# Performance work log

Hardware: AMD Instinct MI355X
Metric: run time of the kernel (lower is better)

The kernel has to match this reference:

```python
import jax, jax.numpy as jnp
import numpy as np

D_MODEL = 1024
HEAD = 16
HEAD_DIM = D_MODEL // HEAD


def setup_inputs() -> dict:
    key = jax.random.key(0)
    ks = jax.random.split(key, 11)
    B, S = 2, 2048
    q = jax.random.normal(ks[0], (B, S, D_MODEL), dtype=jnp.float32)
    k = jax.random.normal(ks[1], (B, S, D_MODEL), dtype=jnp.float32)
    v = jax.random.normal(ks[2], (B, S, D_MODEL), dtype=jnp.float32)
    # nn.Linear-style params: weight [out, in], bias [out]
    w_scale = 1.0 / np.sqrt(D_MODEL)
    def lin(kk):
        kw, kb = jax.random.split(kk)
        W = jax.random.uniform(kw, (D_MODEL, D_MODEL), jnp.float32, -w_scale, w_scale)
        b = jax.random.uniform(kb, (D_MODEL,), jnp.float32, -w_scale, w_scale)
        return W, b
    Wq, bq = lin(ks[3])
    Wk, bk = lin(ks[4])
    Wv, bv = lin(ks[5])
    Wo, bo = lin(ks[6])
    return {"query": q, "key": k, "value": v,
            "Wq": Wq, "bq": bq, "Wk": Wk, "bk": bk,
            "Wv": Wv, "bv": bv, "Wo": Wo, "bo": bo}


def reference(query, key, value, Wq, bq, Wk, bk, Wv, bv, Wo, bo):
    B, S, _ = query.shape
    # QKV projections (nn.Linear: x @ W.T + b)
    q = query @ Wq.T + bq
    k = key @ Wk.T + bk
    v = value @ Wv.T + bv
    # b s (h d) -> b h s d
    def split_heads(t):
        return t.reshape(B, -1, HEAD, HEAD_DIM).transpose(0, 2, 1, 3)
    q, k, v = split_heads(q), split_heads(k), split_heads(v)
    # NOTE: original forward never applies self.scale, and its masked_fill is
    # non-inplace (result discarded), so scores are raw QK^T with no masking.
    scores = jnp.einsum('bhid,bhjd->bhij', q, k)
    attn = jax.nn.softmax(scores, axis=-1)
    out = jnp.einsum('bhij,bhjd->bhid', attn, v)
    # b h s d -> b s (h d)
    out = out.transpose(0, 2, 1, 3).reshape(B, S, D_MODEL)
    # output projection (dropout=0.0)
    return out @ Wo.T + bo
```

## Files before the change

### kernel.cpp

```cpp
#include <hip/hip_runtime.h>
#include <stdint.h>

#define DM   1024
#define SEQ  2048
#define NH   16
#define HD   64
#define SHIFT 14.0f

typedef _Float16 f16;
typedef f16   half8 __attribute__((ext_vector_type(8)));
typedef f16   half4 __attribute__((ext_vector_type(4)));
typedef float f32x4 __attribute__((ext_vector_type(4)));
typedef float f32x16 __attribute__((ext_vector_type(16)));
typedef unsigned int u32;
typedef u32 u32x4 __attribute__((ext_vector_type(4)));

__device__ __forceinline__ void gl_lds16(const void* g, void* l) {
  __builtin_amdgcn_global_load_lds(
      reinterpret_cast<__attribute__((address_space(1))) u32*>(reinterpret_cast<uintptr_t>(g)),
      reinterpret_cast<__attribute__((address_space(3))) u32*>(reinterpret_cast<uintptr_t>(l)),
      16, 0, 0);
}

__device__ __forceinline__ u32 pkrtz(float a, float b) {
  auto h = __builtin_amdgcn_cvt_pkrtz(a, b);
  return __builtin_bit_cast(u32, h);
}

__global__ __launch_bounds__(256) void cast_all(
    const float* __restrict__ q, const float* __restrict__ k, const float* __restrict__ v,
    const float* __restrict__ Wq, const float* __restrict__ Wk,
    const float* __restrict__ Wv, const float* __restrict__ Wo,
    f16* __restrict__ qh, f16* __restrict__ kh, f16* __restrict__ vh,
    f16* __restrict__ Wqh, f16* __restrict__ Wkh, f16* __restrict__ Wvh,
    f16* __restrict__ Woh) {
  int i = blockIdx.x * 256 + threadIdx.x;
  const float* s;
  f16* d;
  int off;
  float sc = 1.0f;
  if (i < 1572864) {
    int sel = i >> 19;
    off = i & 524287;
    s = sel == 0 ? q : sel == 1 ? k : v;
    d = sel == 0 ? qh : sel == 1 ? kh : vh;
  } else {
    int j = i - 1572864;
    int sel = j >> 17;
    off = j & 131071;
    s = sel == 0 ? Wq : sel == 1 ? Wk : sel == 2 ? Wv : Wo;
    d = sel == 0 ? Wqh : sel == 1 ? Wkh : sel == 2 ? Wvh : Woh;
    if (sel == 0) sc = 1.44269504f;
  }
  const float4* s4 = reinterpret_cast<const float4*>(s);
  float4 a = s4[2 * (size_t)off];
  float4 b = s4[2 * (size_t)off + 1];
  half8 o;
  o[0] = (f16)(sc * a.x); o[1] = (f16)(sc * a.y); o[2] = (f16)(sc * a.z); o[3] = (f16)(sc * a.w);
  o[4] = (f16)(sc * b.x); o[5] = (f16)(sc * b.y); o[6] = (f16)(sc * b.z); o[7] = (f16)(sc * b.w);
  *reinterpret_cast<half8*>(d + 8 * (size_t)off) = o;
}

#define XCD_DECODE_N64                                                         \
  int bid = blockIdx.x;                                                        \
  int xcd = bid & 7;                                                           \
  int idx = bid >> 3;                                               \
  int m0 = (xcd * 4 + (idx >> 4)) * 128;                                       \
  int n0 = (idx & 15) * 64;

__global__ __launch_bounds__(512) void gemm_qkv(
    const f16* __restrict__ A0, const f16* __restrict__ A1, const f16* __restrict__ A2,
    const f16* __restrict__ W0, const f16* __restrict__ W1, const f16* __restrict__ W2,
    const float* __restrict__ b0, const float* __restrict__ b1, const float* __restrict__ b2,
    f16* __restrict__ C0, f16* __restrict__ C1, f16* __restrict__ C2) {
  int z = blockIdx.z;
  const f16* A = (z == 0) ? A0 : (z == 1) ? A1 : A2;
  const f16* W = (z == 0) ? W0 : (z == 1) ? W1 : W2;
  const float* bias = (z == 0) ? b0 : (z == 1) ? b1 : b2;

  XCD_DECODE_N64

  __shared__ f16 As[2][128 * 64];
  __shared__ f16 Ws[2][64 * 64];

  int t = threadIdx.x;
  int w = t >> 6, lane = t & 63, lr = lane & 15, lk = lane >> 4;
  int wr = (w >> 1) * 32;
  int wc = (w & 1) * 32;
  int srow = t >> 3;
  int swc = (t & 7) ^ (srow & 7);
  const f16* ga = A + (size_t)(m0 + srow) * DM + swc * 8;
  const f16* gw = W + (size_t)(n0 + srow) * DM + swc * 8;

  f32x4 zero4 = {0.f, 0.f, 0.f, 0.f};
  f32x4 acc[2][2];
#pragma unroll
  for (int mb = 0; mb < 2; ++mb)
#pragma unroll
    for (int nb = 0; nb < 2; ++nb) acc[mb][nb] = zero4;

  gl_lds16(ga,                    &As[0][t * 8]);
  gl_lds16(ga + (size_t)64 * DM,  &As[0][4096 + t * 8]);
  gl_lds16(gw,                    &Ws[0][t * 8]);
  __syncthreads();

  for (int kt = 0; kt < DM / 64; ++kt) {
    int cur = kt & 1;
    if (kt + 1 < DM / 64) {
      int k0 = (kt + 1) * 64;
      gl_lds16(ga + k0,                   &As[cur ^ 1][t * 8]);
      gl_lds16(ga + k0 + (size_t)64 * DM, &As[cur ^ 1][4096 + t * 8]);
      gl_lds16(gw + k0,                   &Ws[cur ^ 1][t * 8]);
    }
#pragma unroll
    for (int ks = 0; ks < 2; ++ks) {
      half8 af[2], wf[2];
#pragma unroll
      for (int mb = 0; mb < 2; ++mb) {
        int R = wr + mb * 16 + lr;
        int c = (ks * 64 + lk * 16) ^ ((lr & 7) << 4);
        af[mb] = *reinterpret_cast<const half8*>(
            reinterpret_cast<const char*>(&As[cur][0]) + R * 128 + c);
      }
#pragma unroll
      for (int nb = 0; nb < 2; ++nb) {
        int R = wc + nb * 16 + lr;
        int c = (ks * 64 + lk * 16) ^ ((lr & 7) << 4);
        wf[nb] = *reinterpret_cast<const half8*>(
            reinterpret_cast<const char*>(&Ws[cur][0]) + R * 128 + c);
      }
#pragma unroll
      for (int mb = 0; mb < 2; ++mb)
#pragma unroll
        for (int nb = 0; nb < 2; ++nb)
          acc[mb][nb] = __builtin_amdgcn_mfma_f32_16x16x32_f16(af[mb], wf[nb], acc[mb][nb], 0, 0, 0);
    }
    __syncthreads();
  }

  float bscale = (z == 0) ? 1.44269504f : 1.0f;
  float bv[2];
#pragma unroll
  for (int nb = 0; nb < 2; ++nb) bv[nb] = bias[n0 + wc + nb * 16 + lr] * bscale;

  int lk4 = lk * 4;
  if (z == 2) {
#pragma unroll
    for (int mb = 0; mb < 2; ++mb)
#pragma unroll
      for (int nb = 0; nb < 2; ++nb) {
        int r0 = m0 + wr + mb * 16 + lk4;
        int c = n0 + wc + nb * 16 + lr;
        int b_ = r0 >> 11, s_ = r0 & 2047;
        int h_ = c >> 6, d_ = c & 63;
        f16* dst = C2 + (((size_t)(b_ * NH + h_) * HD + d_) * SEQ + s_);
        half4 hv;
#pragma unroll
        for (int j = 0; j < 4; ++j) hv[j] = (f16)(acc[mb][nb][j] + bv[nb]);
        *reinterpret_cast<half4*>(dst) = hv;
      }
  } else {
    f16* C = (z == 0) ? C0 : C1;
#pragma unroll
    for (int mb = 0; mb < 2; ++mb)
#pragma unroll
      for (int nb = 0; nb < 2; ++nb)
#pragma unroll
        for (int j = 0; j < 4; ++j) {
          int r = m0 + wr + mb * 16 + lk4 + j;
          int c = n0 + wc + nb * 16 + lr;
          C[(size_t)r * DM + c] = (f16)(acc[mb][nb][j] + bv[nb]);
        }
  }
}

__global__ __launch_bounds__(256) void gemm_out(
    const f16* __restrict__ A, const f16* __restrict__ W,
    const float* __restrict__ bias, float* __restrict__ C) {
  XCD_DECODE_N64

  __shared__ f16 As[2][128 * 64];
  __shared__ f16 Ws[2][64 * 64];
  int t = threadIdx.x;
  int w = t >> 6, lane = t & 63, lr = lane & 15, lk = lane >> 4;
  int wr = (w >> 1) * 64, wc = (w & 1) * 32;
  int rloc = 8 * w + (lane >> 3);
  int swc = (lane & 7) ^ (lane >> 3);
  const f16* ga = A + (size_t)(m0 + rloc) * DM + swc * 8;
  const f16* gw = W + (size_t)(n0 + rloc) * DM + swc * 8;
  f32x4 zero4 = {0.f, 0.f, 0.f, 0.f};
  f32x4 acc[4][2];
#pragma unroll
  for (int mb = 0; mb < 4; ++mb)
#pragma unroll
    for (int nb = 0; nb < 2; ++nb) acc[mb][nb] = zero4;

#pragma unroll
  for (int j = 0; j < 4; ++j)
    gl_lds16(ga + (size_t)(32 * j) * DM, &As[0][j * 2048 + t * 8]);
#pragma unroll
  for (int j = 0; j < 2; ++j)
    gl_lds16(gw + (size_t)(32 * j) * DM, &Ws[0][j * 2048 + t * 8]);
  __syncthreads();

  for (int kt = 0; kt < DM / 64; ++kt) {
    int cur = kt & 1;
    if (kt + 1 < DM / 64) {
      int k0 = (kt + 1) * 64;
#pragma unroll
      for (int j = 0; j < 4; ++j)
        gl_lds16(ga + (size_t)(32 * j) * DM + k0, &As[cur ^ 1][j * 2048 + t * 8]);
#pragma unroll
      for (int j = 0; j < 2; ++j)
        gl_lds16(gw + (size_t)(32 * j) * DM + k0, &Ws[cur ^ 1][j * 2048 + t * 8]);
    }
#pragma unroll
    for (int ks = 0; ks < 2; ++ks) {
      half8 af[4], wf[2];
#pragma unroll
      for (int mb = 0; mb < 4; ++mb) {
        int R = wr + mb * 16 + lr;
        int c = (ks * 64 + lk * 16) ^ ((lr & 7) << 4);
        af[mb] = *reinterpret_cast<const half8*>(
            reinterpret_cast<const char*>(&As[cur][0]) + R * 128 + c);
      }
#pragma unroll
      for (int nb = 0; nb < 2; ++nb) {
        int R = wc + nb * 16 + lr;
        int c = (ks * 64 + lk * 16) ^ ((lr & 7) << 4);
        wf[nb] = *reinterpret_cast<const half8*>(
            reinterpret_cast<const char*>(&Ws[cur][0]) + R * 128 + c);
      }
#pragma unroll
      for (int mb = 0; mb < 4; ++mb)
#pragma unroll
        for (int nb = 0; nb < 2; ++nb)
          acc[mb][nb] = __builtin_amdgcn_mfma_f32_16x16x32_f16(af[mb], wf[nb], acc[mb][nb], 0, 0, 0);
    }
    __syncthreads();
  }

  float bv[2];
#pragma unroll
  for (int nb = 0; nb < 2; ++nb) bv[nb] = bias[n0 + wc + nb * 16 + lr];
  int lk4 = lk * 4;
#pragma unroll
  for (int mb = 0; mb < 4; ++mb)
#pragma unroll
    for (int nb = 0; nb < 2; ++nb)
#pragma unroll
      for (int j = 0; j < 4; ++j) {
        int r = m0 + wr + mb * 16 + lk4 + j;
        int c = n0 + wc + nb * 16 + lr;
        C[(size_t)r * DM + c] = acc[mb][nb][j] + bv[nb];
      }
}

__global__ __launch_bounds__(512) void attn_fwd17(const f16* __restrict__ Qg,
                                                  const f16* __restrict__ Kg,
                                                  const f16* __restrict__ VTg,
                                                  f16* __restrict__ Og) {
  int bid = blockIdx.x;
  int xcd = bid & 7;
  int slot = bid >> 3;
  int qt = slot & 7;
  int gh = slot >> 3;
  int bh = xcd | (gh << 3);
  int b = bh >> 4, h = bh & 15;

  size_t baseq = (size_t)b * SEQ * DM + (size_t)h * HD;
  const f16* Kp = Kg + baseq;
  const f16* VTp = VTg + (size_t)bh * HD * SEQ;

  __shared__ f16 Kl[2][64 * 128];
  __shared__ f16 Vl[2][64 * 128];

  int t = threadIdx.x;
  int w = t >> 6, lane = t & 63;
  int l31 = lane & 31, lh = lane >> 5;
  int vrow = t >> 4, vcb = t & 15;

  int tt = t >> 4;
  int ku = t & 15;
  int ke = (2 * tt) & 15;
  int kx = ku ^ ke;
  int ksel = (kx >> 3) & 1;
  int kcc = ksel ? ((kx ^ 1) & 7) : kx;
  int kvbase = 2 * tt + ksel;
  const f16* gK = Kp + (size_t)kvbase * DM + kcc * 8;
  const f16* gV = VTp + (size_t)vrow * SEQ + ((vcb ^ vrow) & 15) * 8;
  f16* lK = &Kl[0][t * 8];
  f16* lV = &Vl[0][t * 8];
  const int KSTEP = 128 * DM;
  const int VSTEP = 128;
  const int LBK = 64 * 128;
  const int LBV = 64 * 128;

  int qs = qt * 256 + w * 32 + l31;
  const f16* Qrow = Qg + baseq + (size_t)qs * DM;
  half8 qf[4];
#pragma unroll
  for (int s = 0; s < 4; ++s)
    qf[s] = *reinterpret_cast<const half8*>(Qrow + s * 16 + lh * 8);

  auto stage = [&](int kt, int buf) {
    if (t < 256) {
      int ko = kt * KSTEP, vo = kt * VSTEP;
#pragma unroll
      for (int j = 0; j < 4; ++j)
        gl_lds16(gK + ko + (size_t)(32 * j) * DM, lK + buf * LBK + j * 2048);
#pragma unroll
      for (int j = 0; j < 4; ++j)
        gl_lds16(gV + vo + (size_t)(16 * j) * SEQ, lV + buf * LBV + j * 2048);
    }
  };
  auto readKf = [&](int buf, int nbk, int s) -> half8 {
    int kv = nbk * 32 + l31;
    int cc = s * 2 + lh;
    int u = (((kv & 1) << 3) | cc) ^ (kv & 15);
    return *reinterpret_cast<const half8*>(
        reinterpret_cast<const char*>(&Kl[buf][0]) + (kv >> 1) * 256 + (u << 4));
  };
  auto readVf = [&](int buf, int mb, int ks) -> half8 {
    int d = mb * 32 + l31;
    int c = (ks * 32 + lh * 16) ^ ((d & 15) << 4);
    return *reinterpret_cast<const half8*>(
        reinterpret_cast<const char*>(&Vl[buf][0]) + d * 256 + c);
  };

  f32x16 mShift, o0, o1;
#pragma unroll
  for (int i = 0; i < 16; ++i) {
    mShift[i] = -SHIFT;
    o0[i] = 0.f;
    o1[i] = 0.f;
  }
  float l_r = 0.f;

  stage(0, 0);
  __syncthreads();

  const int NT = SEQ / 128;
  for (int kt = 0; kt < NT; ++kt) {
    int cur = kt & 1;
    if (kt + 1 < NT) stage(kt + 1, cur ^ 1);

    __builtin_amdgcn_s_setprio(1);
    half8 k0 = readKf(cur, 0, 0);
    half8 k1 = readKf(cur, 1, 0);
    half8 k2 = readKf(cur, 2, 0);
    half8 k3 = readKf(cur, 3, 0);
    f32x16 s0 = __builtin_amdgcn_mfma_f32_32x32x16_f16(k0, qf[0], mShift, 0, 0, 0);
    f32x16 s1 = __builtin_amdgcn_mfma_f32_32x32x16_f16(k1, qf[0], mShift, 0, 0, 0);
    f32x16 s2 = __builtin_amdgcn_mfma_f32_32x32x16_f16(k2, qf[0], mShift, 0, 0, 0);
    f32x16 s3 = __builtin_amdgcn_mfma_f32_32x32x16_f16(k3, qf[0], mShift, 0, 0, 0);
#pragma unroll
    for (int s = 1; s < 4; ++s) {
      k0 = readKf(cur, 0, s);
      k1 = readKf(cur, 1, s);
      k2 = readKf(cur, 2, s);
      k3 = readKf(cur, 3, s);
      s0 = __builtin_amdgcn_mfma_f32_32x32x16_f16(k0, qf[s], s0, 0, 0, 0);
      s1 = __builtin_amdgcn_mfma_f32_32x32x16_f16(k1, qf[s], s1, 0, 0, 0);
      s2 = __builtin_amdgcn_mfma_f32_32x32x16_f16(k2, qf[s], s2, 0, 0, 0);
      s3 = __builtin_amdgcn_mfma_f32_32x32x16_f16(k3, qf[s], s3, 0, 0, 0);
    }
    __builtin_amdgcn_s_setprio(0);

    float rs0 = 0.f, rs1 = 0.f, rs2 = 0.f, rs3 = 0.f;
#pragma unroll
    for (int i = 0; i < 16; ++i) { s0[i] = __builtin_amdgcn_exp2f(s0[i]); rs0 += s0[i]; }
#pragma unroll
    for (int i = 0; i < 16; ++i) { s1[i] = __builtin_amdgcn_exp2f(s1[i]); rs1 += s1[i]; }
#pragma unroll
    for (int i = 0; i < 16; ++i) { s2[i] = __builtin_amdgcn_exp2f(s2[i]); rs2 += s2[i]; }
#pragma unroll
    for (int i = 0; i < 16; ++i) { s3[i] = __builtin_amdgcn_exp2f(s3[i]); rs3 += s3[i]; }
    l_r += (rs0 + rs1) + (rs2 + rs3);

#define PVSTEP(SP, NBK)                                                        \
    {                                                                          \
      u32 u0 = pkrtz(SP[0], SP[1]);                                            \
      u32 u1 = pkrtz(SP[2], SP[3]);                                            \
      u32 u2 = pkrtz(SP[4], SP[5]);                                            \
      u32 u3 = pkrtz(SP[6], SP[7]);                                            \
      u32 u4 = pkrtz(SP[8], SP[9]);                                            \
      u32 u5 = pkrtz(SP[10], SP[11]);                                          \
      u32 u6 = pkrtz(SP[12], SP[13]);                                          \
      u32 u7 = pkrtz(SP[14], SP[15]);                                          \
      asm volatile("v_permlane32_swap_b32 %0, %1" : "+v"(u0), "+v"(u2));       \
      asm volatile("v_permlane32_swap_b32 %0, %1" : "+v"(u1), "+v"(u3));       \
      asm volatile("v_permlane32_swap_b32 %0, %1" : "+v"(u4), "+v"(u6));       \
      asm volatile("v_permlane32_swap_b32 %0, %1" : "+v"(u5), "+v"(u7));       \
      u32x4 w0 = {u0, u1, u2, u3};                                             \
      u32x4 w1 = {u4, u5, u6, u7};                                             \
      half8 pa0 = __builtin_bit_cast(half8, w0);                               \
      half8 pa1 = __builtin_bit_cast(half8, w1);                               \
      half8 va = readVf(cur, 0, 2 * NBK);                                      \
      half8 vb = readVf(cur, 1, 2 * NBK);                                      \
      __builtin_amdgcn_s_setprio(1);                                           \
      o0 = __builtin_amdgcn_mfma_f32_32x32x16_f16(va, pa0, o0, 0, 0, 0);       \
      o1 = __builtin_amdgcn_mfma_f32_32x32x16_f16(vb, pa0, o1, 0, 0, 0);       \
      __builtin_amdgcn_s_setprio(0);                                           \
      va = readVf(cur, 0, 2 * NBK + 1);                                        \
      vb = readVf(cur, 1, 2 * NBK + 1);                                        \
      __builtin_amdgcn_s_setprio(1);                                           \
      o0 = __builtin_amdgcn_mfma_f32_32x32x16_f16(va, pa1, o0, 0, 0, 0);       \
      o1 = __builtin_amdgcn_mfma_f32_32x32x16_f16(vb, pa1, o1, 0, 0, 0);       \
      __builtin_amdgcn_s_setprio(0);                                           \
    }
    PVSTEP(s0, 0)
    PVSTEP(s1, 1)
    PVSTEP(s2, 2)
    PVSTEP(s3, 3)
#undef PVSTEP

    __syncthreads();
  }

  float l_all = l_r + __shfl_xor(l_r, 32);
  float inv = 1.0f / l_all;
  f16* Orow = Og + baseq + (size_t)qs * DM;
#pragma unroll
  for (int mb = 0; mb < 2; ++mb) {
    const f32x16& oo = mb ? o1 : o0;
#pragma unroll
    for (int rq = 0; rq < 4; ++rq) {
      half4 hv;
      hv[0] = (f16)(oo[4 * rq + 0] * inv);
      hv[1] = (f16)(oo[4 * rq + 1] * inv);
      hv[2] = (f16)(oo[4 * rq + 2] * inv);
      hv[3] = (f16)(oo[4 * rq + 3] * inv);
      *reinterpret_cast<half4*>(Orow + mb * 32 + 8 * rq + 4 * lh) = hv;
    }
  }
}

extern "C" void kernel_launch(void* const* d_in, const int* in_sizes, int n_in,
                              void* d_out, int out_size, void* d_ws, size_t ws_size,
                              hipStream_t stream) {
  (void)in_sizes; (void)n_in; (void)out_size; (void)ws_size;
  const float* q  = (const float*)d_in[0];
  const float* k  = (const float*)d_in[1];
  const float* v  = (const float*)d_in[2];
  const float* Wq = (const float*)d_in[3];
  const float* bq = (const float*)d_in[4];
  const float* Wk = (const float*)d_in[5];
  const float* bk = (const float*)d_in[6];
  const float* Wv = (const float*)d_in[7];
  const float* bv = (const float*)d_in[8];
  const float* Wo = (const float*)d_in[9];
  const float* bo = (const float*)d_in[10];
  float* out = (float*)d_out;

  char* ws = (char*)d_ws;
  const size_t MB = 1u << 20;
  f16* qh  = (f16*)(ws + 0 * MB);
  f16* kh  = (f16*)(ws + 8 * MB);
  f16* vh  = (f16*)(ws + 16 * MB);
  f16* Wqh = (f16*)(ws + 24 * MB);
  f16* Wkh = (f16*)(ws + 26 * MB);
  f16* Wvh = (f16*)(ws + 28 * MB);
  f16* Woh = (f16*)(ws + 30 * MB);
  f16* Qp  = (f16*)(ws + 32 * MB);
  f16* Kp  = (f16*)(ws + 40 * MB);
  f16* Vtp = (f16*)(ws + 48 * MB);
  f16* At  = (f16*)(ws + 56 * MB);

  cast_all<<<8192, 256, 0, stream>>>(q, k, v, Wq, Wk, Wv, Wo,
                                     qh, kh, vh, Wqh, Wkh, Wvh, Woh);
  gemm_qkv<<<dim3(512, 1, 3), 512, 0, stream>>>(qh, kh, vh, Wqh, Wkh, Wvh,
                                                bq, bk, bv, Qp, Kp, Vtp);
  attn_fwd17<<<256, 512, 0, stream>>>(Qp, Kp, Vtp, At);
  gemm_out<<<512, 256, 0, stream>>>(At, Woh, bo, out);
}
```

Before: 106.7 us.

## Fuse activation fp32-to-fp16 cast into QKV GEMM A-tile loads

Drops the separate cast of the q/k/v activations. The QKV GEMM now loads fp32 activations straight from global memory into registers, converts them to fp16 with cvt_pkrtz, and writes them into swizzled LDS after the MFMA work for each step. The goal is to remove the write and re-read of the fp16 activation copy, about 24 MB of extra traffic plus one kernel's worth of work. In exchange, the A tiles move from async global-to-LDS loads to register loads. Each A tile is also re-read as fp32 by every N-tile block, so that GEMM's input traffic doubles.

```diff
diff --git a/kernel.cpp b/kernel.cpp
--- a/kernel.cpp
+++ b/kernel.cpp
@@ -27,31 +27,17 @@
   return __builtin_bit_cast(u32, h);
 }
 
-__global__ __launch_bounds__(256) void cast_all(
-    const float* __restrict__ q, const float* __restrict__ k, const float* __restrict__ v,
+__global__ __launch_bounds__(256) void cast_w(
     const float* __restrict__ Wq, const float* __restrict__ Wk,
     const float* __restrict__ Wv, const float* __restrict__ Wo,
-    f16* __restrict__ qh, f16* __restrict__ kh, f16* __restrict__ vh,
     f16* __restrict__ Wqh, f16* __restrict__ Wkh, f16* __restrict__ Wvh,
     f16* __restrict__ Woh) {
   int i = blockIdx.x * 256 + threadIdx.x;
-  const float* s;
-  f16* d;
-  int off;
-  float sc = 1.0f;
-  if (i < 1572864) {
-    int sel = i >> 19;
-    off = i & 524287;
-    s = sel == 0 ? q : sel == 1 ? k : v;
-    d = sel == 0 ? qh : sel == 1 ? kh : vh;
-  } else {
-    int j = i - 1572864;
-    int sel = j >> 17;
-    off = j & 131071;
-    s = sel == 0 ? Wq : sel == 1 ? Wk : sel == 2 ? Wv : Wo;
-    d = sel == 0 ? Wqh : sel == 1 ? Wkh : sel == 2 ? Wvh : Woh;
-    if (sel == 0) sc = 1.44269504f;
-  }
+  int sel = i >> 17;
+  int off = i & 131071;
+  const float* s = sel == 0 ? Wq : sel == 1 ? Wk : sel == 2 ? Wv : Wo;
+  f16* d = sel == 0 ? Wqh : sel == 1 ? Wkh : sel == 2 ? Wvh : Woh;
+  float sc = (sel == 0) ? 1.44269504f : 1.0f;
   const float4* s4 = reinterpret_cast<const float4*>(s);
   float4 a = s4[2 * (size_t)off];
   float4 b = s4[2 * (size_t)off + 1];
@@ -69,12 +55,12 @@
   int n0 = (idx & 15) * 64;
 
 __global__ __launch_bounds__(512) void gemm_qkv(
-    const f16* __restrict__ A0, const f16* __restrict__ A1, const f16* __restrict__ A2,
+    const float* __restrict__ A0, const float* __restrict__ A1, const float* __restrict__ A2,
     const f16* __restrict__ W0, const f16* __restrict__ W1, const f16* __restrict__ W2,
     const float* __restrict__ b0, const float* __restrict__ b1, const float* __restrict__ b2,
     f16* __restrict__ C0, f16* __restrict__ C1, f16* __restrict__ C2) {
   int z = blockIdx.z;
-  const f16* A = (z == 0) ? A0 : (z == 1) ? A1 : A2;
+  const float* A = (z == 0) ? A0 : (z == 1) ? A1 : A2;
   const f16* W = (z == 0) ? W0 : (z == 1) ? W1 : W2;
   const float* bias = (z == 0) ? b0 : (z == 1) ? b1 : b2;
 
@@ -89,7 +75,7 @@
   int wc = (w & 1) * 32;
   int srow = t >> 3;
   int swc = (t & 7) ^ (srow & 7);
-  const f16* ga = A + (size_t)(m0 + srow) * DM + swc * 8;
+  const float* gaf = A + (size_t)(m0 + srow) * DM + swc * 8;
   const f16* gw = W + (size_t)(n0 + srow) * DM + swc * 8;
 
   f32x4 zero4 = {0.f, 0.f, 0.f, 0.f};
@@ -99,18 +85,30 @@
 #pragma unroll
     for (int nb = 0; nb < 2; ++nb) acc[mb][nb] = zero4;
 
-  gl_lds16(ga,                    &As[0][t * 8]);
-  gl_lds16(ga + (size_t)64 * DM,  &As[0][4096 + t * 8]);
-  gl_lds16(gw,                    &Ws[0][t * 8]);
+  {
+    float4 a0 = *reinterpret_cast<const float4*>(gaf);
+    float4 a1 = *reinterpret_cast<const float4*>(gaf + 4);
+    float4 c0 = *reinterpret_cast<const float4*>(gaf + (size_t)64 * DM);
+    float4 c1 = *reinterpret_cast<const float4*>(gaf + (size_t)64 * DM + 4);
+    gl_lds16(gw, &Ws[0][t * 8]);
+    u32x4 p0 = {pkrtz(a0.x, a0.y), pkrtz(a0.z, a0.w), pkrtz(a1.x, a1.y), pkrtz(a1.z, a1.w)};
+    u32x4 p1 = {pkrtz(c0.x, c0.y), pkrtz(c0.z, c0.w), pkrtz(c1.x, c1.y), pkrtz(c1.z, c1.w)};
+    *reinterpret_cast<u32x4*>(&As[0][t * 8]) = p0;
+    *reinterpret_cast<u32x4*>(&As[0][4096 + t * 8]) = p1;
+  }
   __syncthreads();
 
   for (int kt = 0; kt < DM / 64; ++kt) {
     int cur = kt & 1;
-    if (kt + 1 < DM / 64) {
+    bool pre = (kt + 1 < DM / 64);
+    float4 a0, a1, c0, c1;
+    if (pre) {
       int k0 = (kt + 1) * 64;
-      gl_lds16(ga + k0,                   &As[cur ^ 1][t * 8]);
-      gl_lds16(ga + k0 + (size_t)64 * DM, &As[cur ^ 1][4096 + t * 8]);
-      gl_lds16(gw + k0,                   &Ws[cur ^ 1][t * 8]);
+      a0 = *reinterpret_cast<const float4*>(gaf + k0);
+      a1 = *reinterpret_cast<const float4*>(gaf + k0 + 4);
+      c0 = *reinterpret_cast<const float4*>(gaf + k0 + (size_t)64 * DM);
+      c1 = *reinterpret_cast<const float4*>(gaf + k0 + (size_t)64 * DM + 4);
+      gl_lds16(gw + k0, &Ws[cur ^ 1][t * 8]);
     }
 #pragma unroll
     for (int ks = 0; ks < 2; ++ks) {
@@ -134,6 +132,12 @@
 #pragma unroll
         for (int nb = 0; nb < 2; ++nb)
           acc[mb][nb] = __builtin_amdgcn_mfma_f32_16x16x32_f16(af[mb], wf[nb], acc[mb][nb], 0, 0, 0);
+    }
+    if (pre) {
+      u32x4 p0 = {pkrtz(a0.x, a0.y), pkrtz(a0.z, a0.w), pkrtz(a1.x, a1.y), pkrtz(a1.z, a1.w)};
+      u32x4 p1 = {pkrtz(c0.x, c0.y), pkrtz(c0.z, c0.w), pkrtz(c1.x, c1.y), pkrtz(c1.z, c1.w)};
+      *reinterpret_cast<u32x4*>(&As[cur ^ 1][t * 8]) = p0;
+      *reinterpret_cast<u32x4*>(&As[cur ^ 1][4096 + t * 8]) = p1;
     }
     __syncthreads();
   }
@@ -455,9 +459,6 @@
 
   char* ws = (char*)d_ws;
   const size_t MB = 1u << 20;
-  f16* qh  = (f16*)(ws + 0 * MB);
-  f16* kh  = (f16*)(ws + 8 * MB);
-  f16* vh  = (f16*)(ws + 16 * MB);
   f16* Wqh = (f16*)(ws + 24 * MB);
   f16* Wkh = (f16*)(ws + 26 * MB);
   f16* Wvh = (f16*)(ws + 28 * MB);
@@ -467,9 +468,8 @@
   f16* Vtp = (f16*)(ws + 48 * MB);
   f16* At  = (f16*)(ws + 56 * MB);
 
-  cast_all<<<8192, 256, 0, stream>>>(q, k, v, Wq, Wk, Wv, Wo,
-                                     qh, kh, vh, Wqh, Wkh, Wvh, Woh);
-  gemm_qkv<<<dim3(512, 1, 3), 512, 0, stream>>>(qh, kh, vh, Wqh, Wkh, Wvh,
+  cast_w<<<2048, 256, 0, stream>>>(Wq, Wk, Wv, Wo, Wqh, Wkh, Wvh, Woh);
+  gemm_qkv<<<dim3(512, 1, 3), 512, 0, stream>>>(q, k, v, Wqh, Wkh, Wvh,
                                                 bq, bk, bv, Qp, Kp, Vtp);
   attn_fwd17<<<256, 512, 0, stream>>>(Qp, Kp, Vtp, At);
   gemm_out<<<512, 256, 0, stream>>>(At, Woh, bo, out);
```

New measurement: 115.4 us. 8.1% more time.
